# Kernel optimization log

Measured on AMD Instinct MI355X. Metric: run time of the kernel, lower is better.

The kernel has to match this reference:

```python
import jax, jax.numpy as jnp
import numpy as np

N = 50000
E = 800000
F_IN = 2      # num_node_features
H = 2         # heads
C = 64        # embedding_size (per-head out channels)
HID = 128     # hidden_size (message dim)
B = 512       # number of messages
NEG_SLOPE = 0.2


def gatv2_conv(x, src, dst, edge_attr, Wl, bl, Wr, br, We, att, bias):
    # x: [N, F_IN]; src/dst: [E]; edge_attr: [E, 1]
    n = x.shape[0]
    xl = (x @ Wl + bl).reshape(n, H, C)   # source transform (lin_l)
    xr = (x @ Wr + br).reshape(n, H, C)   # target transform (lin_r)
    ea = (edge_attr @ We).reshape(-1, H, C)
    m = xl[src] + xr[dst] + ea                      # [E, H, C]
    e = jnp.where(m > 0, m, NEG_SLOPE * m)          # LeakyReLU
    score = jnp.einsum('ehc,hc->eh', e, att)        # [E, H]
    # scatter-softmax over incoming edges of each target node
    smax = jax.ops.segment_max(score, dst, num_segments=n)
    smax = jnp.where(jnp.isfinite(smax), smax, 0.0)
    ex = jnp.exp(score - smax[dst])
    denom = jax.ops.segment_sum(ex, dst, num_segments=n)
    alpha = ex / (denom[dst] + 1e-16)               # [E, H]
    out = jax.ops.segment_sum(xl[src] * alpha[:, :, None], dst, num_segments=n)
    return out.reshape(n, H * C) + bias


def setup_inputs() -> dict:
    key = jax.random.key(0)
    ks = jax.random.split(key, 20)
    s = 0.1
    inp = {
        'message': jax.random.normal(ks[0], (B, HID), jnp.float32),
        'x': jax.random.normal(ks[1], (N, F_IN), jnp.float32),
        'edge_index': jax.random.randint(ks[2], (2, E), 0, N, jnp.int32),
        'edge_attr': jax.random.normal(ks[3], (E, 1), jnp.float32),
    }
    def conv_params(base):
        return {
            'Wl': jax.random.normal(ks[base], (F_IN, H * C)) * s,
            'bl': jnp.zeros((H * C,), jnp.float32),
            'Wr': jax.random.normal(ks[base + 1], (F_IN, H * C)) * s,
            'br': jnp.zeros((H * C,), jnp.float32),
            'We': jax.random.normal(ks[base + 2], (1, H * C)) * s,
            'att': jax.random.normal(ks[base + 3], (H, C)) * s,
            'bias': jnp.zeros((H * C,), jnp.float32),
        }
    p1 = {k + '1': v for k, v in conv_params(4).items()}
    p2 = {k + '2': v for k, v in conv_params(8).items()}
    inp.update(p1)
    inp.update(p2)
    inp['Wfc'] = jax.random.normal(ks[12], (HID, H * C)) * s
    inp['bfc'] = jnp.zeros((H * C,), jnp.float32)
    return inp


def reference(message, x, edge_index, edge_attr,
              Wl1, bl1, Wr1, br1, We1, att1, bias1,
              Wl2, bl2, Wr2, br2, We2, att2, bias2,
              Wfc, bfc):
    src, dst = edge_index[0], edge_index[1]
    # conv1 output is computed but unused in the original forward (conv2 takes x again)
    h1 = jax.nn.relu(gatv2_conv(x, src, dst, edge_attr, Wl1, bl1, Wr1, br1, We1, att1, bias1))
    h = jax.nn.relu(gatv2_conv(x, src, dst, edge_attr, Wl2, bl2, Wr2, br2, We2, att2, bias2))
    msg = jnp.concatenate([message, message], axis=0)      # [2B, HID]
    msg_emb = msg @ Wfc + bfc                              # [2B, H*C]
    dot = h @ msg_emb.T                                    # [N, 2B]
    return jax.nn.softmax(dot, axis=0)
```

## Files before the change

kernel.cpp:

```cpp
#include <hip/hip_runtime.h>
#include <hip/hip_bf16.h>
#include <hip/hip_cooperative_groups.h>

namespace cg = cooperative_groups;

#define N_NODES 50000
#define N_EDGES 800000
#define BLK     256
#define NTILES  782
#define NB_SCAN 196
#define SMEM_SZ 34816

typedef __attribute__((ext_vector_type(8))) short short8;
typedef __attribute__((ext_vector_type(16))) float f32x16;

struct Params {
  const float* msg; const float* x; const int* ei; const float* ea;
  const float* Wl; const float* bl; const float* Wr; const float* br;
  const float* We; const float* att; const float* bias;
  const float* Wfc; const float* bfc;
  float4* rec; float* nodeF;
  __hip_bfloat16* me_hi; __hip_bfloat16* me_lo;
  int* cnt; float* colsum; int* offs; int* cursor; int* bsum;
  float* w6;
  float* dout;
};

template<int PASS>
__device__ __forceinline__ void mfma_tile(const Params& P, int tile, char* SMEM)
{
  short8* Bt   = (short8*)SMEM;
  float*  xp   = (float*)SMEM;
  float*  rcol = (float*)(SMEM + 32768);
  float*  colacc = (float*)(SMEM + 32768);

  const int tid = threadIdx.x;
  const int l = tid & 63, w = tid >> 6;
  const int rt = w >> 1, ct = w & 1;
  const int lrow = l & 31, lhalf = l >> 5;
  const int m0 = tile * 64;
  const int row = m0 + rt * 32 + lrow;

  float c0a = 0.f, c0b = 0.f, c0d = 0.f, c1a = 0.f, c1b = 0.f, c1d = 0.f;
  bool live = row < N_NODES;
  if (live) {
    const float* nf = P.nodeF + (size_t)row * 8;
    float4 n0 = *(const float4*)nf;
    float4 n1 = *(const float4*)(nf + 4);
    float r0 = 1.0f / (n0.x + 1e-16f), r1 = 1.0f / (n0.w + 1e-16f);
    c0a = n0.y * r0; c0b = n0.z * r0; c0d = n0.x * r0;
    c1a = n1.x * r1; c1b = n1.y * r1; c1d = n0.w * r1;
  }
  short8 a_hi[8], a_lo[8];
  #pragma unroll
  for (int ks = 0; ks < 8; ++ks) {
    int k0 = ks * 16 + lhalf * 8;
    float ca = (ks < 4) ? c0a : c1a;
    float cbv = (ks < 4) ? c0b : c1b;
    float cd = (ks < 4) ? c0d : c1d;
    float wA[8], wB[8], wC[8], wD[8];
    *(float4*)&wA[0] = *(const float4*)(P.Wl + k0);
    *(float4*)&wA[4] = *(const float4*)(P.Wl + k0 + 4);
    *(float4*)&wB[0] = *(const float4*)(P.Wl + 128 + k0);
    *(float4*)&wB[4] = *(const float4*)(P.Wl + 128 + k0 + 4);
    *(float4*)&wC[0] = *(const float4*)(P.bl + k0);
    *(float4*)&wC[4] = *(const float4*)(P.bl + k0 + 4);
    *(float4*)&wD[0] = *(const float4*)(P.bias + k0);
    *(float4*)&wD[4] = *(const float4*)(P.bias + k0 + 4);
    short8 hi8, lo8;
    #pragma unroll
    for (int j = 0; j < 8; ++j) {
      float v = ca * wA[j] + cbv * wB[j] + cd * wC[j] + wD[j];
      v = (live && v > 0.f) ? v : 0.f;
      __hip_bfloat16 hb = __float2bfloat16(v);
      float rem = v - __bfloat162float(hb);
      __hip_bfloat16 lb = __float2bfloat16(rem);
      short hs, ls;
      __builtin_memcpy(&hs, &hb, 2);
      __builtin_memcpy(&ls, &lb, 2);
      hi8[j] = hs; lo8[j] = ls;
    }
    a_hi[ks] = hi8; a_lo[ks] = lo8;
  }

  const int colB = ct * 32 + lrow;

  for (int cb = 0; cb < 8; ++cb) {
    __syncthreads();
    #pragma unroll
    for (int q = 0; q < 8; ++q) {
      int lin = q * 256 + tid;
      int s = lin & 1023;
      int col = s >> 4, ku = s & 15;
      int slot = ku * 64 + (col ^ ku);
      size_t gb = ((size_t)(cb * 64 + col) << 7) + ku * 8;
      if (lin < 1024) Bt[slot] = *(const short8*)(P.me_hi + gb);
      else            Bt[1024 + slot] = *(const short8*)(P.me_lo + gb);
    }
    __syncthreads();

    f32x16 acc = {0.f};
    #pragma unroll
    for (int ks = 0; ks < 8; ++ks) {
      int ku = ks * 2 + lhalf;
      int slot = ku * 64 + (colB ^ ku);
      short8 bh = Bt[slot];
      short8 blo = Bt[1024 + slot];
      acc = __builtin_amdgcn_mfma_f32_32x32x16_bf16(a_hi[ks], bh, acc, 0, 0, 0);
      acc = __builtin_amdgcn_mfma_f32_32x32x16_bf16(a_lo[ks], bh, acc, 0, 0, 0);
      acc = __builtin_amdgcn_mfma_f32_32x32x16_bf16(a_hi[ks], blo, acc, 0, 0, 0);
    }

    if (PASS == 0) {
      float csum = 0.f;
      #pragma unroll
      for (int i = 0; i < 16; ++i) {
        int grow = m0 + rt * 32 + (i & 3) + 8 * (i >> 2) + 4 * lhalf;
        csum += (grow < N_NODES) ? __expf(acc[i]) : 0.f;
      }
      csum += __shfl_xor(csum, 32);
      if (l < 32)
        atomicAdd(&colacc[cb * 64 + ct * 32 + l], csum);
    } else {
      __syncthreads();
      #pragma unroll
      for (int i = 0; i < 16; ++i) {
        int rl = rt * 32 + (i & 3) + 8 * (i >> 2) + 4 * lhalf;
        xp[rl * 68 + ct * 32 + lrow] = __expf(acc[i]);
      }
      __syncthreads();
      #pragma unroll
      for (int q = 0; q < 4; ++q) {
        int fid = q * 256 + tid;
        int rl = fid >> 4, c4 = fid & 15;
        int grow = m0 + rl;
        float4 v = *(float4*)&xp[rl * 68 + c4 * 4];
        float4 s = *(const float4*)&rcol[cb * 64 + c4 * 4];
        v.x *= s.x; v.y *= s.y; v.z *= s.z; v.w *= s.w;
        if (grow < N_NODES) {
          *(float4*)&P.dout[(size_t)grow * 1024 + cb * 64 + c4 * 4] = v;
          *(float4*)&P.dout[(size_t)grow * 1024 + 512 + cb * 64 + c4 * 4] = v;
        }
      }
    }
  }
}

__global__ __launch_bounds__(BLK, 3) void k_all(Params P)
{
  cg::grid_group gg = cg::this_grid();
  __shared__ __align__(16) char SMEM[SMEM_SZ];
  const int b = blockIdx.x, t = threadIdx.x;
  const int G = gridDim.x;

  if (b < 256) {
    float* mrow = (float*)SMEM;
    int r = 2 * b + (t >> 7);
    int col = t & 127;
    mrow[t] = P.msg[r * 128 + col];
    __syncthreads();
    int base = (t >> 7) * 128;
    float acc = P.bfc[col];
    #pragma unroll 8
    for (int k = 0; k < 128; ++k) acc = fmaf(mrow[base + k], P.Wfc[k * 128 + col], acc);
    __hip_bfloat16 hi = __float2bfloat16(acc);
    P.me_hi[r * 128 + col] = hi;
    P.me_lo[r * 128 + col] = __float2bfloat16(acc - __bfloat162float(hi));
  } else if (b < 454) {
    int i = (b - 256) * 256 + t;
    if (i < N_NODES + 512) P.cnt[i] = 0;
  } else if (b == 454 && t < 128) {
    int k = t;
    float4 a = make_float4(P.bl[k] + P.br[k], P.Wl[k], P.Wl[128 + k], P.Wr[k]);
    float4 c = make_float4(P.Wr[128 + k], P.We[k], P.att[k], 0.f);
    *(float4*)&P.w6[k * 8] = a;
    *(float4*)&P.w6[k * 8 + 4] = c;
  }
  gg.sync();

  for (int e = b * BLK + t; e < N_EDGES; e += G * BLK)
    atomicAdd(&P.cnt[P.ei[N_EDGES + e]], 1);
  gg.sync();

  const int CH = (N_NODES + G - 1) / G;

  {
    int* sh = (int*)SMEM;
    int base = b * CH;
    if (t < 128) sh[t] = 0;
    __syncthreads();
    int v = 0;
    if (t < 128 && t < CH && base + t < N_NODES) { v = P.cnt[base + t]; sh[t] = v; }
    __syncthreads();
    #pragma unroll
    for (int off = 1; off < 128; off <<= 1) {
      int u = (t < 128 && t >= off) ? sh[t - off] : 0;
      __syncthreads();
      if (t < 128) sh[t] += u;
      __syncthreads();
    }
    if (t < 128 && t < CH && base + t < N_NODES) P.offs[base + t] = sh[t] - v;
    if (t == 0) P.bsum[b] = sh[127];
  }
  gg.sync();

  {
    int* eb = (int*)SMEM;
    int* s3 = eb + 1024;
    const int nb = G >> 8;
    int xv[4];
    int ssum = 0;
    for (int j = 0; j < nb; ++j) { xv[j] = P.bsum[nb * t + j]; ssum += xv[j]; }
    s3[t] = ssum;
    __syncthreads();
    #pragma unroll
    for (int off = 1; off < 256; off <<= 1) {
      int u = (t >= off) ? s3[t - off] : 0;
      __syncthreads();
      s3[t] += u;
      __syncthreads();
    }
    int p = t ? s3[t - 1] : 0;
    for (int j = 0; j < nb; ++j) { eb[nb * t + j] = p; p += xv[j]; }
    __syncthreads();
    int pb = eb[b];
    int base = b * CH;
    if (t < CH && base + t < N_NODES) {
      int o = P.offs[base + t] + pb;
      P.offs[base + t] = o;
      P.cursor[base + t] = o;
    }
    if (b == 0 && t == 0) P.offs[N_NODES] = N_EDGES;
  }
  gg.sync();

  {
    const float4* W4 = (const float4*)P.w6;
    for (int e = b * BLK + t; e < N_EDGES; e += G * BLK) {
      int s = P.ei[e], d = P.ei[N_EDGES + e];
      float x0s = P.x[2*s], x1s = P.x[2*s+1];
      float x0d = P.x[2*d], x1d = P.x[2*d+1];
      float av = P.ea[e];
      float s0 = 0.f, s1 = 0.f;
      #pragma unroll 8
      for (int k = 0; k < 64; ++k) {
        float4 a = W4[2*k], c = W4[2*k+1];
        float m = a.x;
        m = fmaf(x0s, a.y, m);
        m = fmaf(x1s, a.z, m);
        m = fmaf(x0d, a.w, m);
        m = fmaf(x1d, c.x, m);
        m = fmaf(av,  c.y, m);
        s0 = fmaf(fmaxf(m, 0.2f * m), c.z, s0);
      }
      #pragma unroll 8
      for (int k = 64; k < 128; ++k) {
        float4 a = W4[2*k], c = W4[2*k+1];
        float m = a.x;
        m = fmaf(x0s, a.y, m);
        m = fmaf(x1s, a.z, m);
        m = fmaf(x0d, a.w, m);
        m = fmaf(x1d, c.x, m);
        m = fmaf(av,  c.y, m);
        s1 = fmaf(fmaxf(m, 0.2f * m), c.z, s1);
      }
      int pos = atomicAdd(&P.cursor[d], 1);
      P.rec[pos] = make_float4(s0, s1, x0s, x1s);
    }
  }
  gg.sync();

  {
    int n = b * BLK + t;
    if (n < N_NODES) {
      int a = P.offs[n], bb = P.offs[n + 1];
      float D0 = 0.f, A00 = 0.f, A10 = 0.f;
      float D1 = 0.f, A01 = 0.f, A11 = 0.f;
      for (int i = a; i < bb; ++i) {
        float4 r = P.rec[i];
        float e0 = __expf(r.x);
        float e1 = __expf(r.y);
        D0 += e0; A00 += e0 * r.z; A10 += e0 * r.w;
        D1 += e1; A01 += e1 * r.z; A11 += e1 * r.w;
      }
      float* nf = P.nodeF + (size_t)n * 8;
      nf[0] = D0; nf[1] = A00; nf[2] = A10;
      nf[3] = D1; nf[4] = A01; nf[5] = A11;
    }
  }
  gg.sync();

  {
    float* colacc = (float*)(SMEM + 32768);
    colacc[t] = 0.f; colacc[t + 256] = 0.f;
    __syncthreads();
    for (int tile = b; tile < NTILES; tile += G)
      mfma_tile<0>(P, tile, SMEM);
    __syncthreads();
    atomicAdd(&P.colsum[t], colacc[t]);
    atomicAdd(&P.colsum[t + 256], colacc[t + 256]);
  }
  gg.sync();

  {
    float* rcol = (float*)(SMEM + 32768);
    rcol[t] = 1.0f / P.colsum[t];
    rcol[t + 256] = 1.0f / P.colsum[t + 256];
    __syncthreads();
    for (int tile = b; tile < NTILES; tile += G)
      mfma_tile<1>(P, tile, SMEM);
  }
}

__global__ __launch_bounds__(256) void k_zero(int* __restrict__ buf)
{
  int i = blockIdx.x * 256 + threadIdx.x;
  if (i < N_NODES + 512) buf[i] = 0;
}

__global__ __launch_bounds__(256) void k_hist(
    const int* __restrict__ ei, int* __restrict__ cnt)
{
  int e = blockIdx.x * 256 + threadIdx.x;
  if (e >= N_EDGES) return;
  atomicAdd(&cnt[ei[N_EDGES + e]], 1);
}

__global__ __launch_bounds__(256) void k_scan1(
    const int* __restrict__ cnt, int* __restrict__ offs, int* __restrict__ bsum)
{
  __shared__ int sh[256];
  int b = blockIdx.x, t = threadIdx.x;
  int i = b * 256 + t;
  int v = (i < N_NODES) ? cnt[i] : 0;
  sh[t] = v;
  __syncthreads();
  #pragma unroll
  for (int off = 1; off < 256; off <<= 1) {
    int u = (t >= off) ? sh[t - off] : 0;
    __syncthreads();
    sh[t] += u;
    __syncthreads();
  }
  if (i < N_NODES) offs[i] = sh[t] - v;
  if (t == 255) bsum[b] = sh[255];
}

__global__ __launch_bounds__(256) void k_scan2(int* __restrict__ bsum)
{
  __shared__ int sh[256];
  int t = threadIdx.x;
  int v = (t < NB_SCAN) ? bsum[t] : 0;
  sh[t] = v;
  __syncthreads();
  #pragma unroll
  for (int off = 1; off < 256; off <<= 1) {
    int u = (t >= off) ? sh[t - off] : 0;
    __syncthreads();
    sh[t] += u;
    __syncthreads();
  }
  if (t < NB_SCAN) bsum[t] = sh[t] - v;
}

__global__ __launch_bounds__(256) void k_scan3(
    int* __restrict__ offs, const int* __restrict__ bsum, int* __restrict__ cursor)
{
  int b = blockIdx.x, t = threadIdx.x;
  int i = b * 256 + t;
  if (i < N_NODES) {
    int o = offs[i] + bsum[b];
    offs[i] = o;
    cursor[i] = o;
  }
  if (b == 0 && t == 0) offs[N_NODES] = N_EDGES;
}

__global__ void k_w6(Params P)
{
  int k = threadIdx.x;
  if (k < 128) {
    float4 a = make_float4(P.bl[k] + P.br[k], P.Wl[k], P.Wl[128 + k], P.Wr[k]);
    float4 c = make_float4(P.Wr[128 + k], P.We[k], P.att[k], 0.f);
    *(float4*)&P.w6[k * 8] = a;
    *(float4*)&P.w6[k * 8 + 4] = c;
  }
}

__global__ __launch_bounds__(256) void k_scatter(Params P)
{
  int e = blockIdx.x * 256 + threadIdx.x;
  if (e >= N_EDGES) return;
  const float4* W4 = (const float4*)P.w6;
  int s = P.ei[e], d = P.ei[N_EDGES + e];
  float x0s = P.x[2*s], x1s = P.x[2*s+1];
  float x0d = P.x[2*d], x1d = P.x[2*d+1];
  float av = P.ea[e];
  float s0 = 0.f, s1 = 0.f;
  #pragma unroll 8
  for (int k = 0; k < 64; ++k) {
    float4 a = W4[2*k], c = W4[2*k+1];
    float m = a.x;
    m = fmaf(x0s, a.y, m);
    m = fmaf(x1s, a.z, m);
    m = fmaf(x0d, a.w, m);
    m = fmaf(x1d, c.x, m);
    m = fmaf(av,  c.y, m);
    s0 = fmaf(fmaxf(m, 0.2f * m), c.z, s0);
  }
  #pragma unroll 8
  for (int k = 64; k < 128; ++k) {
    float4 a = W4[2*k], c = W4[2*k+1];
    float m = a.x;
    m = fmaf(x0s, a.y, m);
    m = fmaf(x1s, a.z, m);
    m = fmaf(x0d, a.w, m);
    m = fmaf(x1d, c.x, m);
    m = fmaf(av,  c.y, m);
    s1 = fmaf(fmaxf(m, 0.2f * m), c.z, s1);
  }
  int pos = atomicAdd(&P.cursor[d], 1);
  P.rec[pos] = make_float4(s0, s1, x0s, x1s);
}

__global__ __launch_bounds__(256) void k_gather(Params P)
{
  int n = blockIdx.x * 256 + threadIdx.x;
  if (n >= N_NODES) return;
  int a = P.offs[n], b = P.offs[n + 1];
  float D0 = 0.f, A00 = 0.f, A10 = 0.f;
  float D1 = 0.f, A01 = 0.f, A11 = 0.f;
  for (int i = a; i < b; ++i) {
    float4 r = P.rec[i];
    float e0 = __expf(r.x);
    float e1 = __expf(r.y);
    D0 += e0; A00 += e0 * r.z; A10 += e0 * r.w;
    D1 += e1; A01 += e1 * r.z; A11 += e1 * r.w;
  }
  float* nf = P.nodeF + (size_t)n * 8;
  nf[0] = D0; nf[1] = A00; nf[2] = A10;
  nf[3] = D1; nf[4] = A01; nf[5] = A11;
}

__global__ __launch_bounds__(128) void k_fc(Params P)
{
  int j = blockIdx.x, k = threadIdx.x;
  __shared__ float mrow[128];
  mrow[k] = P.msg[j*128 + k];
  __syncthreads();
  float acc = P.bfc[k];
  #pragma unroll 8
  for (int t = 0; t < 128; ++t) acc = fmaf(mrow[t], P.Wfc[t*128 + k], acc);
  __hip_bfloat16 hi = __float2bfloat16(acc);
  P.me_hi[j*128 + k] = hi;
  P.me_lo[j*128 + k] = __float2bfloat16(acc - __bfloat162float(hi));
}

template<int PASS>
__global__ __launch_bounds__(256, 3) void k_mfma(Params P)
{
  __shared__ __align__(16) char SMEM[SMEM_SZ];
  int tid = threadIdx.x;
  if (PASS == 0) {
    float* colacc = (float*)(SMEM + 32768);
    colacc[tid] = 0.f; colacc[tid + 256] = 0.f;
    __syncthreads();
    mfma_tile<0>(P, blockIdx.x, SMEM);
    __syncthreads();
    atomicAdd(&P.colsum[tid], colacc[tid]);
    atomicAdd(&P.colsum[tid + 256], colacc[tid + 256]);
  } else {
    float* rcol = (float*)(SMEM + 32768);
    rcol[tid] = 1.0f / P.colsum[tid];
    rcol[tid + 256] = 1.0f / P.colsum[tid + 256];
    __syncthreads();
    mfma_tile<1>(P, blockIdx.x, SMEM);
  }
}

extern "C" void kernel_launch(void* const* d_in, const int* in_sizes, int n_in,
                              void* d_out, int out_size, void* d_ws, size_t ws_size,
                              hipStream_t stream)
{
  Params P;
  P.msg = (const float*)d_in[0];
  P.x   = (const float*)d_in[1];
  P.ei  = (const int*)d_in[2];
  P.ea  = (const float*)d_in[3];
  P.Wl   = (const float*)d_in[11];
  P.bl   = (const float*)d_in[12];
  P.Wr   = (const float*)d_in[13];
  P.br   = (const float*)d_in[14];
  P.We   = (const float*)d_in[15];
  P.att  = (const float*)d_in[16];
  P.bias = (const float*)d_in[17];
  P.Wfc  = (const float*)d_in[18];
  P.bfc  = (const float*)d_in[19];

  char* p = (char*)d_ws;
  P.rec = (float4*)p;                    p += (size_t)N_EDGES * 16;
  P.nodeF = (float*)p;                   p += (size_t)N_NODES * 8 * 4;
  P.me_hi = (__hip_bfloat16*)p;          p += 512 * 128 * 2;
  P.me_lo = (__hip_bfloat16*)p;          p += 512 * 128 * 2;
  P.cnt = (int*)p;                       p += (size_t)N_NODES * 4;
  P.colsum = (float*)p;                  p += 512 * 4;
  P.offs = (int*)p;                      p += (size_t)(N_NODES + 1) * 4;
  P.cursor = (int*)p;                    p += (size_t)N_NODES * 4;
  P.bsum = (int*)p;                      p += 1024 * 4;
  P.w6 = (float*)p;                      p += 128 * 8 * 4;
  P.dout = (float*)d_out;

  int maxBlk = 0;
  hipError_t qerr = hipOccupancyMaxActiveBlocksPerMultiprocessor(&maxBlk, k_all, BLK, 0);
  if (qerr == hipSuccess && maxBlk >= 2) {
    int g = (maxBlk >= 3) ? 768 : 512;
    void* args[] = { &P };
    hipError_t lerr = hipLaunchCooperativeKernel((void*)k_all, dim3(g), dim3(BLK),
                                                 args, 0, stream);
    if (lerr == hipSuccess) return;
  }

  k_zero<<<(N_NODES + 512 + 255) / 256, 256, 0, stream>>>(P.cnt);
  k_hist<<<(N_EDGES + 255) / 256, 256, 0, stream>>>(P.ei, P.cnt);
  k_scan1<<<NB_SCAN, 256, 0, stream>>>(P.cnt, P.offs, P.bsum);
  k_scan2<<<1, 256, 0, stream>>>(P.bsum);
  k_scan3<<<NB_SCAN, 256, 0, stream>>>(P.offs, P.bsum, P.cursor);
  k_w6<<<1, 128, 0, stream>>>(P);
  k_scatter<<<(N_EDGES + 255) / 256, 256, 0, stream>>>(P);
  k_gather<<<(N_NODES + 255) / 256, 256, 0, stream>>>(P);
  k_fc<<<512, 128, 0, stream>>>(P);
  k_mfma<0><<<NTILES, 256, 0, stream>>>(P);
  k_mfma<1><<<NTILES, 256, 0, stream>>>(P);
}
```

Measured before the change: 234.4 us.

## Assign each block one column block and loop over row tiles in MFMA passes

Each block is now assigned a single 64-column slice of the message embedding, which it loads into shared memory once, and then iterates over row tiles. Previously every tile reloaded all eight column slices, with barriers around each load. The trade-off is that the A-operand construction from nodeF and the bf16 hi/lo split are now redone for every tile in each column group, so that work is repeated eight times. The per-column reciprocal is folded into the exp store, and colsum partials are reduced per column block before one global atomic.

```diff
diff --git a/kernel.cpp b/kernel.cpp
--- a/kernel.cpp
+++ b/kernel.cpp
@@ -9,7 +9,9 @@
 #define BLK     256
 #define NTILES  782
 #define NB_SCAN 196
-#define SMEM_SZ 34816
+#define XP_OFF  32768
+#define CS_OFF  (32768 + 17408)
+#define SMEM_SZ (CS_OFF + 256)
 
 typedef __attribute__((ext_vector_type(8))) short short8;
 typedef __attribute__((ext_vector_type(16))) float f32x16;
@@ -27,77 +29,81 @@
 };
 
 template<int PASS>
-__device__ __forceinline__ void mfma_tile(const Params& P, int tile, char* SMEM)
-{
-  short8* Bt   = (short8*)SMEM;
-  float*  xp   = (float*)SMEM;
-  float*  rcol = (float*)(SMEM + 32768);
-  float*  colacc = (float*)(SMEM + 32768);
+__device__ __forceinline__ void mfma_pass(const Params& P, int cb, int rg, int nrg,
+                                          char* SMEM)
+{
+  short8* Bt     = (short8*)SMEM;
+  float*  xp     = (float*)(SMEM + XP_OFF);
+  float*  cshare = (float*)(SMEM + CS_OFF);
 
   const int tid = threadIdx.x;
   const int l = tid & 63, w = tid >> 6;
   const int rt = w >> 1, ct = w & 1;
   const int lrow = l & 31, lhalf = l >> 5;
-  const int m0 = tile * 64;
-  const int row = m0 + rt * 32 + lrow;
-
-  float c0a = 0.f, c0b = 0.f, c0d = 0.f, c1a = 0.f, c1b = 0.f, c1d = 0.f;
-  bool live = row < N_NODES;
-  if (live) {
-    const float* nf = P.nodeF + (size_t)row * 8;
-    float4 n0 = *(const float4*)nf;
-    float4 n1 = *(const float4*)(nf + 4);
-    float r0 = 1.0f / (n0.x + 1e-16f), r1 = 1.0f / (n0.w + 1e-16f);
-    c0a = n0.y * r0; c0b = n0.z * r0; c0d = n0.x * r0;
-    c1a = n1.x * r1; c1b = n1.y * r1; c1d = n0.w * r1;
-  }
-  short8 a_hi[8], a_lo[8];
+  const int colB = ct * 32 + lrow;
+
+  if (tid < 64)
+    cshare[tid] = (PASS == 0) ? 0.f : (1.0f / P.colsum[cb * 64 + tid]);
+
   #pragma unroll
-  for (int ks = 0; ks < 8; ++ks) {
-    int k0 = ks * 16 + lhalf * 8;
-    float ca = (ks < 4) ? c0a : c1a;
-    float cbv = (ks < 4) ? c0b : c1b;
-    float cd = (ks < 4) ? c0d : c1d;
-    float wA[8], wB[8], wC[8], wD[8];
-    *(float4*)&wA[0] = *(const float4*)(P.Wl + k0);
-    *(float4*)&wA[4] = *(const float4*)(P.Wl + k0 + 4);
-    *(float4*)&wB[0] = *(const float4*)(P.Wl + 128 + k0);
-    *(float4*)&wB[4] = *(const float4*)(P.Wl + 128 + k0 + 4);
-    *(float4*)&wC[0] = *(const float4*)(P.bl + k0);
-    *(float4*)&wC[4] = *(const float4*)(P.bl + k0 + 4);
-    *(float4*)&wD[0] = *(const float4*)(P.bias + k0);
-    *(float4*)&wD[4] = *(const float4*)(P.bias + k0 + 4);
-    short8 hi8, lo8;
+  for (int q = 0; q < 8; ++q) {
+    int lin = q * 256 + tid;
+    int s = lin & 1023;
+    int col = s >> 4, ku = s & 15;
+    int slot = ku * 64 + (col ^ ku);
+    size_t gb = ((size_t)(cb * 64 + col) << 7) + ku * 8;
+    if (lin < 1024) Bt[slot] = *(const short8*)(P.me_hi + gb);
+    else            Bt[1024 + slot] = *(const short8*)(P.me_lo + gb);
+  }
+  __syncthreads();
+
+  const float rS = (PASS == 1) ? cshare[colB] : 0.f;
+
+  for (int tile = rg; tile < NTILES; tile += nrg) {
+    const int m0 = tile * 64;
+    const int row = m0 + rt * 32 + lrow;
+
+    float c0a = 0.f, c0b = 0.f, c0d = 0.f, c1a = 0.f, c1b = 0.f, c1d = 0.f;
+    bool live = row < N_NODES;
+    if (live) {
+      const float* nf = P.nodeF + (size_t)row * 8;
+      float4 n0 = *(const float4*)nf;
+      float4 n1 = *(const float4*)(nf + 4);
+      float r0 = 1.0f / (n0.x + 1e-16f), r1 = 1.0f / (n0.w + 1e-16f);
+      c0a = n0.y * r0; c0b = n0.z * r0; c0d = n0.x * r0;
+      c1a = n1.x * r1; c1b = n1.y * r1; c1d = n0.w * r1;
+    }
+    short8 a_hi[8], a_lo[8];
     #pragma unroll
-    for (int j = 0; j < 8; ++j) {
-      float v = ca * wA[j] + cbv * wB[j] + cd * wC[j] + wD[j];
-      v = (live && v > 0.f) ? v : 0.f;
-      __hip_bfloat16 hb = __float2bfloat16(v);
-      float rem = v - __bfloat162float(hb);
-      __hip_bfloat16 lb = __float2bfloat16(rem);
-      short hs, ls;
-      __builtin_memcpy(&hs, &hb, 2);
-      __builtin_memcpy(&ls, &lb, 2);
-      hi8[j] = hs; lo8[j] = ls;
-    }
-    a_hi[ks] = hi8; a_lo[ks] = lo8;
-  }
-
-  const int colB = ct * 32 + lrow;
-
-  for (int cb = 0; cb < 8; ++cb) {
-    __syncthreads();
-    #pragma unroll
-    for (int q = 0; q < 8; ++q) {
-      int lin = q * 256 + tid;
-      int s = lin & 1023;
-      int col = s >> 4, ku = s & 15;
-      int slot = ku * 64 + (col ^ ku);
-      size_t gb = ((size_t)(cb * 64 + col) << 7) + ku * 8;
-      if (lin < 1024) Bt[slot] = *(const short8*)(P.me_hi + gb);
-      else            Bt[1024 + slot] = *(const short8*)(P.me_lo + gb);
-    }
-    __syncthreads();
+    for (int ks = 0; ks < 8; ++ks) {
+      int k0 = ks * 16 + lhalf * 8;
+      float ca = (ks < 4) ? c0a : c1a;
+      float cbv = (ks < 4) ? c0b : c1b;
+      float cd = (ks < 4) ? c0d : c1d;
+      float wA[8], wB[8], wC[8], wD[8];
+      *(float4*)&wA[0] = *(const float4*)(P.Wl + k0);
+      *(float4*)&wA[4] = *(const float4*)(P.Wl + k0 + 4);
+      *(float4*)&wB[0] = *(const float4*)(P.Wl + 128 + k0);
+      *(float4*)&wB[4] = *(const float4*)(P.Wl + 128 + k0 + 4);
+      *(float4*)&wC[0] = *(const float4*)(P.bl + k0);
+      *(float4*)&wC[4] = *(const float4*)(P.bl + k0 + 4);
+      *(float4*)&wD[0] = *(const float4*)(P.bias + k0);
+      *(float4*)&wD[4] = *(const float4*)(P.bias + k0 + 4);
+      short8 hi8, lo8;
+      #pragma unroll
+      for (int j = 0; j < 8; ++j) {
+        float v = ca * wA[j] + cbv * wB[j] + cd * wC[j] + wD[j];
+        v = (live && v > 0.f) ? v : 0.f;
+        __hip_bfloat16 hb = __float2bfloat16(v);
+        float rem = v - __bfloat162float(hb);
+        __hip_bfloat16 lb = __float2bfloat16(rem);
+        short hs, ls;
+        __builtin_memcpy(&hs, &hb, 2);
+        __builtin_memcpy(&ls, &lb, 2);
+        hi8[j] = hs; lo8[j] = ls;
+      }
+      a_hi[ks] = hi8; a_lo[ks] = lo8;
+    }
 
     f32x16 acc = {0.f};
     #pragma unroll
@@ -119,14 +125,13 @@
         csum += (grow < N_NODES) ? __expf(acc[i]) : 0.f;
       }
       csum += __shfl_xor(csum, 32);
-      if (l < 32)
-        atomicAdd(&colacc[cb * 64 + ct * 32 + l], csum);
+      if (l < 32) atomicAdd(&cshare[ct * 32 + l], csum);
     } else {
       __syncthreads();
       #pragma unroll
       for (int i = 0; i < 16; ++i) {
         int rl = rt * 32 + (i & 3) + 8 * (i >> 2) + 4 * lhalf;
-        xp[rl * 68 + ct * 32 + lrow] = __expf(acc[i]);
+        xp[rl * 68 + colB] = __expf(acc[i]) * rS;
       }
       __syncthreads();
       #pragma unroll
@@ -134,15 +139,18 @@
         int fid = q * 256 + tid;
         int rl = fid >> 4, c4 = fid & 15;
         int grow = m0 + rl;
-        float4 v = *(float4*)&xp[rl * 68 + c4 * 4];
-        float4 s = *(const float4*)&rcol[cb * 64 + c4 * 4];
-        v.x *= s.x; v.y *= s.y; v.z *= s.z; v.w *= s.w;
         if (grow < N_NODES) {
+          float4 v = *(float4*)&xp[rl * 68 + c4 * 4];
           *(float4*)&P.dout[(size_t)grow * 1024 + cb * 64 + c4 * 4] = v;
           *(float4*)&P.dout[(size_t)grow * 1024 + 512 + cb * 64 + c4 * 4] = v;
         }
       }
     }
+  }
+
+  if (PASS == 0) {
+    __syncthreads();
+    if (tid < 64) atomicAdd(&P.colsum[cb * 64 + tid], cshare[tid]);
   }
 }
 
@@ -290,26 +298,10 @@
   }
   gg.sync();
 
-  {
-    float* colacc = (float*)(SMEM + 32768);
-    colacc[t] = 0.f; colacc[t + 256] = 0.f;
-    __syncthreads();
-    for (int tile = b; tile < NTILES; tile += G)
-      mfma_tile<0>(P, tile, SMEM);
-    __syncthreads();
-    atomicAdd(&P.colsum[t], colacc[t]);
-    atomicAdd(&P.colsum[t + 256], colacc[t + 256]);
-  }
-  gg.sync();
-
-  {
-    float* rcol = (float*)(SMEM + 32768);
-    rcol[t] = 1.0f / P.colsum[t];
-    rcol[t + 256] = 1.0f / P.colsum[t + 256];
-    __syncthreads();
-    for (int tile = b; tile < NTILES; tile += G)
-      mfma_tile<1>(P, tile, SMEM);
-  }
+  mfma_pass<0>(P, b & 7, b >> 3, G >> 3, SMEM);
+  gg.sync();
+
+  mfma_pass<1>(P, b & 7, b >> 3, G >> 3, SMEM);
 }
 
 __global__ __launch_bounds__(256) void k_zero(int* __restrict__ buf)
@@ -460,22 +452,7 @@
 __global__ __launch_bounds__(256, 3) void k_mfma(Params P)
 {
   __shared__ __align__(16) char SMEM[SMEM_SZ];
-  int tid = threadIdx.x;
-  if (PASS == 0) {
-    float* colacc = (float*)(SMEM + 32768);
-    colacc[tid] = 0.f; colacc[tid + 256] = 0.f;
-    __syncthreads();
-    mfma_tile<0>(P, blockIdx.x, SMEM);
-    __syncthreads();
-    atomicAdd(&P.colsum[tid], colacc[tid]);
-    atomicAdd(&P.colsum[tid + 256], colacc[tid + 256]);
-  } else {
-    float* rcol = (float*)(SMEM + 32768);
-    rcol[tid] = 1.0f / P.colsum[tid];
-    rcol[tid + 256] = 1.0f / P.colsum[tid + 256];
-    __syncthreads();
-    mfma_tile<1>(P, blockIdx.x, SMEM);
-  }
+  mfma_pass<PASS>(P, blockIdx.x, blockIdx.y, gridDim.y, SMEM);
 }
 
 extern "C" void kernel_launch(void* const* d_in, const int* in_sizes, int n_in,
@@ -529,6 +506,6 @@
   k_scatter<<<(N_EDGES + 255) / 256, 256, 0, stream>>>(P);
   k_gather<<<(N_NODES + 255) / 256, 256, 0, stream>>>(P);
   k_fc<<<512, 128, 0, stream>>>(P);
-  k_mfma<0><<<NTILES, 256, 0, stream>>>(P);
-  k_mfma<1><<<NTILES, 256, 0, stream>>>(P);
-}
+  k_mfma<0><<<dim3(8, 96), 256, 0, stream>>>(P);
+  k_mfma<1><<<dim3(8, 96), 256, 0, stream>>>(P);
+}
```

New measurement: 348.8 us. 1.49x slower.
